# Kernel tuning notes

Hardware: AMD Instinct MI355X
Metric: run time of the kernel (lower is better)

The kernel has to match this reference:

```python
import jax, jax.numpy as jnp
import numpy as np

N = 250_000
E = 8_000_000
EPS = 1e-5


def _bn(x, gamma, beta):
    # BatchNorm1d in training mode: batch stats over dim 0, biased variance
    mu = x.mean(axis=0)
    var = x.var(axis=0)
    return (x - mu) * jax.lax.rsqrt(var + EPS) * gamma + beta


def setup_inputs() -> dict:
    key = jax.random.key(0)
    ks = jax.random.split(key, 24)
    f32 = jnp.float32
    inp = {
        'pos': jax.random.normal(ks[0], (N, 2), f32),
        'vel': jax.random.normal(ks[1], (N, 2), f32),
        'edge_index': jax.random.randint(ks[2], (2, E), 0, N, jnp.int32),
        'lin_in_w': jax.random.normal(ks[3], (4, 4), f32) * 0.5,
        'lin_in_b': jax.random.normal(ks[4], (4,), f32) * 0.1,
        'msg_w1': jax.random.normal(ks[5], (8, 8), f32) * 0.35,
        'msg_b1': jax.random.normal(ks[6], (8,), f32) * 0.1,
        'msg_g1': jax.random.uniform(ks[7], (8,), f32, 0.5, 1.5),
        'msg_be1': jax.random.normal(ks[8], (8,), f32) * 0.1,
        'msg_w2': jax.random.normal(ks[9], (8, 4), f32) * 0.35,
        'msg_b2': jax.random.normal(ks[10], (4,), f32) * 0.1,
        'msg_g2': jax.random.uniform(ks[11], (4,), f32, 0.5, 1.5),
        'msg_be2': jax.random.normal(ks[12], (4,), f32) * 0.1,
        'upd_w1': jax.random.normal(ks[13], (8, 8), f32) * 0.35,
        'upd_b1': jax.random.normal(ks[14], (8,), f32) * 0.1,
        'upd_g1': jax.random.uniform(ks[15], (8,), f32, 0.5, 1.5),
        'upd_be1': jax.random.normal(ks[16], (8,), f32) * 0.1,
        'upd_w2': jax.random.normal(ks[17], (8, 4), f32) * 0.35,
        'upd_b2': jax.random.normal(ks[18], (4,), f32) * 0.1,
        'upd_g2': jax.random.uniform(ks[19], (4,), f32, 0.5, 1.5),
        'upd_be2': jax.random.normal(ks[20], (4,), f32) * 0.1,
        'pred_w': jax.random.normal(ks[21], (4, 2), f32) * 0.5,
        'pred_b': jax.random.normal(ks[22], (2,), f32) * 0.1,
    }
    return inp


def reference(pos, vel, edge_index,
              lin_in_w, lin_in_b,
              msg_w1, msg_b1, msg_g1, msg_be1,
              msg_w2, msg_b2, msg_g2, msg_be2,
              upd_w1, upd_b1, upd_g1, upd_be1,
              upd_w2, upd_b2, upd_g2, upd_be2,
              pred_w, pred_b):
    n = pos.shape[0]
    # input projection: h = lin_in(cat(pos, vel))  -> [N, 4]
    h = jnp.concatenate([pos, vel], axis=-1) @ lin_in_w + lin_in_b

    # PyG source_to_target: j = source = edge_index[0], i = target = edge_index[1]
    src, dst = edge_index[0], edge_index[1]
    h_i = h[dst]  # [E, 4]
    h_j = h[src]  # [E, 4]

    # message MLP on cat(h_i, h_j): Linear->BN->Tanh->Linear->BN->Tanh
    m = jnp.concatenate([h_i, h_j], axis=-1)            # [E, 8]
    m = jnp.tanh(_bn(m @ msg_w1 + msg_b1, msg_g1, msg_be1))
    m = jnp.tanh(_bn(m @ msg_w2 + msg_b2, msg_g2, msg_be2))  # [E, 4]

    # zero out messages where h_i == h_j exactly (self-like edges)
    zero_diff = jnp.all(h_i == h_j, axis=1)             # [E]
    m = jnp.where(zero_diff[:, None], 0.0, m)

    # aggregate: scatter-add on first half, scatter-mean on second half
    add_out = jax.ops.segment_sum(m[:, :2], dst, num_segments=n)   # [N, 2]
    sum_out = jax.ops.segment_sum(m[:, 2:], dst, num_segments=n)   # [N, 2]
    cnt = jax.ops.segment_sum(jnp.ones((m.shape[0],), m.dtype), dst, num_segments=n)
    mean_out = sum_out / jnp.maximum(cnt, 1.0)[:, None]
    aggr = jnp.concatenate([add_out, mean_out], axis=1)  # [N, 4]

    # update MLP on cat(h, aggr)
    u = jnp.concatenate([h, aggr], axis=-1)              # [N, 8]
    u = jnp.tanh(_bn(u @ upd_w1 + upd_b1, upd_g1, upd_be1))
    u = jnp.tanh(_bn(u @ upd_w2 + upd_b2, upd_g2, upd_be2))  # [N, 4]

    return u @ pred_w + pred_b                           # [N, 2]
```

## Files before the change

kernel.cpp:

```cpp
#include <hip/hip_runtime.h>

#define EPSBN 1e-5f
#define NB 512
#define GB 256
#define CAP 18000

typedef float vf4 __attribute__((ext_vector_type(4)));
typedef _Float16 vh8 __attribute__((ext_vector_type(8)));
typedef _Float16 vh4 __attribute__((ext_vector_type(4)));
typedef unsigned int uint32;

__device__ __forceinline__ float ftanh(float x) {
    float e = __expf(2.0f * x);
    return 1.0f - 2.0f * __builtin_amdgcn_rcpf(e + 1.0f);
}

__device__ __forceinline__ float wave_sum(float v) {
#pragma unroll
    for (int off = 32; off > 0; off >>= 1) v += __shfl_down(v, off);
    return v;
}

__device__ __forceinline__ void z1_of(const float4 hi, const float4 hj,
                                      const float* __restrict__ w, const float* __restrict__ b,
                                      float* z) {
#pragma unroll
    for (int j = 0; j < 8; ++j) {
        z[j] = b[j]
             + hi.x * w[0 * 8 + j] + hi.y * w[1 * 8 + j] + hi.z * w[2 * 8 + j] + hi.w * w[3 * 8 + j]
             + hj.x * w[4 * 8 + j] + hj.y * w[5 * 8 + j] + hj.z * w[6 * 8 + j] + hj.w * w[7 * 8 + j];
    }
}

__device__ __forceinline__ void mat8x4(const float* u, const float* w,
                                       const float* b, float* z) {
#pragma unroll
    for (int c = 0; c < 4; ++c) {
        float t = b[c];
#pragma unroll
        for (int k = 0; k < 8; ++k) t += u[k] * w[k * 4 + c];
        z[c] = t;
    }
}

__device__ __forceinline__ void mat8x8(const float* u, const float* __restrict__ w,
                                       const float* __restrict__ b, float* z) {
#pragma unroll
    for (int j = 0; j < 8; ++j) {
        float t = b[j];
#pragma unroll
        for (int k = 0; k < 8; ++k) t += u[k] * w[k * 8 + j];
        z[j] = t;
    }
}

template <int NV, int NW>
__device__ __forceinline__ void block_reduce_atomics(float* a, float* __restrict__ sums) {
    __shared__ float red[NV * NW];
    int wid = threadIdx.x >> 6, lane = threadIdx.x & 63;
#pragma unroll
    for (int i = 0; i < NV; ++i) {
        float v = wave_sum(a[i]);
        if (lane == 0) red[i * NW + wid] = v;
    }
    __syncthreads();
    if (threadIdx.x < NV) {
        float v = 0.f;
#pragma unroll
        for (int k = 0; k < NW; ++k) v += red[threadIdx.x * NW + k];
        atomicAdd(&sums[threadIdx.x], v);
    }
}

__device__ __forceinline__ void fin_lds(const float* __restrict__ sums,
                                        const float* __restrict__ g, const float* __restrict__ be,
                                        int d, float inv, float* out) {
    int j = threadIdx.x;
    if (j < d) {
        float mu = sums[j] * inv;
        float var = sums[d + j] * inv - mu * mu;
        float s = g[j] * rsqrtf(var + EPSBN);
        out[j] = s;
        out[d + j] = be[j] - mu * s;
    }
    __syncthreads();
}

__device__ __forceinline__ void stats1_edge(float4 hi, float4 hj,
                                            const float* __restrict__ w1, const float* __restrict__ b1,
                                            float* a) {
    float z[8];
    z1_of(hi, hj, w1, b1, z);
#pragma unroll
    for (int j = 0; j < 8; ++j) { a[j] += z[j]; a[8 + j] += z[j] * z[j]; }
}

__device__ __forceinline__ vf4 z2_edge(float4 hi, float4 hj,
                                       const float* __restrict__ w1, const float* __restrict__ b1,
                                       const float* ss1,
                                       const float* __restrict__ w2, const float* __restrict__ b2) {
    float z[8], m1[8], z2[4];
    z1_of(hi, hj, w1, b1, z);
#pragma unroll
    for (int j = 0; j < 8; ++j) m1[j] = ftanh(z[j] * ss1[j] + ss1[8 + j]);
    mat8x4(m1, w2, b2, z2);
    vf4 r = {z2[0], z2[1], z2[2], z2[3]};
    return r;
}

__device__ __forceinline__ void stats2_edge(float4 hi, float4 hj,
                                            const float* __restrict__ w1, const float* __restrict__ b1,
                                            const float* ss1,
                                            const float* __restrict__ w2, const float* __restrict__ b2,
                                            float* a) {
    vf4 q = z2_edge(hi, hj, w1, b1, ss1, w2, b2);
    a[0] += q.x; a[4] += q.x * q.x;
    a[1] += q.y; a[5] += q.y * q.y;
    a[2] += q.z; a[6] += q.z * q.z;
    a[3] += q.w; a[7] += q.w * q.w;
}

__device__ __forceinline__ void m1_ofh(vf4 ziA, vf4 ziB, vh8 zjh, float* m1) {
    m1[0] = ftanh(ziA.x + (float)zjh[0]); m1[1] = ftanh(ziA.y + (float)zjh[1]);
    m1[2] = ftanh(ziA.z + (float)zjh[2]); m1[3] = ftanh(ziA.w + (float)zjh[3]);
    m1[4] = ftanh(ziB.x + (float)zjh[4]); m1[5] = ftanh(ziB.y + (float)zjh[5]);
    m1[6] = ftanh(ziB.z + (float)zjh[6]); m1[7] = ftanh(ziB.w + (float)zjh[7]);
}

__global__ __launch_bounds__(256) void k_h(const float* __restrict__ pos, const float* __restrict__ vel,
                                           const float* __restrict__ w, const float* __restrict__ b,
                                           float4* __restrict__ h, int n) {
    int i = blockIdx.x * blockDim.x + threadIdx.x;
    if (i >= n) return;
    float2 p = ((const float2*)pos)[i];
    float2 v = ((const float2*)vel)[i];
    float o[4];
#pragma unroll
    for (int d = 0; d < 4; ++d)
        o[d] = b[d] + p.x * w[0 * 4 + d] + p.y * w[1 * 4 + d] + v.x * w[2 * 4 + d] + v.y * w[3 * 4 + d];
    h[i] = make_float4(o[0], o[1], o[2], o[3]);
}

__global__ __launch_bounds__(256) void k_zt(const float4* __restrict__ h,
                                            const float* __restrict__ w1, const float* __restrict__ b1,
                                            vf4* __restrict__ zi, vf4* __restrict__ zj, int n) {
    int i = blockIdx.x * blockDim.x + threadIdx.x;
    if (i >= n) return;
    float4 hv = h[i];
    float zi8[8], zj8[8];
#pragma unroll
    for (int j = 0; j < 8; ++j) {
        zi8[j] = hv.x * w1[0 * 8 + j] + hv.y * w1[1 * 8 + j] + hv.z * w1[2 * 8 + j] + hv.w * w1[3 * 8 + j];
        zj8[j] = b1[j]
               + hv.x * w1[4 * 8 + j] + hv.y * w1[5 * 8 + j] + hv.z * w1[6 * 8 + j] + hv.w * w1[7 * 8 + j];
    }
    vf4 a = {zi8[0], zi8[1], zi8[2], zi8[3]};
    vf4 b_ = {zi8[4], zi8[5], zi8[6], zi8[7]};
    vf4 c = {zj8[0], zj8[1], zj8[2], zj8[3]};
    vf4 d = {zj8[4], zj8[5], zj8[6], zj8[7]};
    zi[2 * (size_t)i] = a; zi[2 * (size_t)i + 1] = b_;
    zj[2 * (size_t)i] = c; zj[2 * (size_t)i + 1] = d;
}

__global__ __launch_bounds__(256) void k_fold(vf4* __restrict__ zi, const vf4* __restrict__ zj,
                                              vh8* __restrict__ zjH,
                                              const float* __restrict__ sums1,
                                              const float* __restrict__ g1, const float* __restrict__ be1,
                                              float invE, int n) {
    __shared__ float ss1[16];
    fin_lds(sums1, g1, be1, 8, invE, ss1);
    int i = blockIdx.x * blockDim.x + threadIdx.x;
    if (i >= n) return;
    vf4 a = zi[2 * (size_t)i], b = zi[2 * (size_t)i + 1];
    a.x *= ss1[0]; a.y *= ss1[1]; a.z *= ss1[2]; a.w *= ss1[3];
    b.x *= ss1[4]; b.y *= ss1[5]; b.z *= ss1[6]; b.w *= ss1[7];
    zi[2 * (size_t)i] = a; zi[2 * (size_t)i + 1] = b;
    vf4 c = zj[2 * (size_t)i], d = zj[2 * (size_t)i + 1];
    vh8 hpk;
    hpk[0] = (_Float16)(c.x * ss1[0] + ss1[8]);
    hpk[1] = (_Float16)(c.y * ss1[1] + ss1[9]);
    hpk[2] = (_Float16)(c.z * ss1[2] + ss1[10]);
    hpk[3] = (_Float16)(c.w * ss1[3] + ss1[11]);
    hpk[4] = (_Float16)(d.x * ss1[4] + ss1[12]);
    hpk[5] = (_Float16)(d.y * ss1[5] + ss1[13]);
    hpk[6] = (_Float16)(d.z * ss1[6] + ss1[14]);
    hpk[7] = (_Float16)(d.w * ss1[7] + ss1[15]);
    zjH[i] = hpk;
}

__global__ __launch_bounds__(1024, 1) void k_cnt(const int* __restrict__ idx, const float4* __restrict__ h,
                                                 const float* __restrict__ w1, const float* __restrict__ b1,
                                                 uint32* __restrict__ cntmat, float* __restrict__ sums,
                                                 int E_, int T) {
    __shared__ uint32 hist[NB];
    for (int b = threadIdx.x; b < NB; b += 1024) hist[b] = 0;
    float a[16];
#pragma unroll
    for (int i = 0; i < 16; ++i) a[i] = 0.f;
    __syncthreads();
    int lo = blockIdx.x * T, hi2 = min(E_, lo + T);
    for (int e0 = lo + 4 * threadIdx.x; e0 < hi2; e0 += 4096) {
        int m = min(4, hi2 - e0);
        if (m == 4) {
            int s0 = __builtin_nontemporal_load(idx + e0);
            int s1 = __builtin_nontemporal_load(idx + e0 + 1);
            int s2 = __builtin_nontemporal_load(idx + e0 + 2);
            int s3 = __builtin_nontemporal_load(idx + e0 + 3);
            int d0 = __builtin_nontemporal_load(idx + E_ + e0);
            int d1 = __builtin_nontemporal_load(idx + E_ + e0 + 1);
            int d2 = __builtin_nontemporal_load(idx + E_ + e0 + 2);
            int d3 = __builtin_nontemporal_load(idx + E_ + e0 + 3);
            float4 hi0 = h[d0], hj0 = h[s0];
            float4 hi1 = h[d1], hj1 = h[s1];
            float4 hi2 = h[d2], hj2 = h[s2];
            float4 hi3 = h[d3], hj3 = h[s3];
            atomicAdd(&hist[d0 >> 9], 1u);
            atomicAdd(&hist[d1 >> 9], 1u);
            atomicAdd(&hist[d2 >> 9], 1u);
            atomicAdd(&hist[d3 >> 9], 1u);
            stats1_edge(hi0, hj0, w1, b1, a);
            stats1_edge(hi1, hj1, w1, b1, a);
            stats1_edge(hi2, hj2, w1, b1, a);
            stats1_edge(hi3, hj3, w1, b1, a);
        } else {
            for (int k = 0; k < m; ++k) {
                int s = __builtin_nontemporal_load(idx + e0 + k);
                int d = __builtin_nontemporal_load(idx + E_ + e0 + k);
                float4 hi = h[d], hj = h[s];
                atomicAdd(&hist[d >> 9], 1u);
                stats1_edge(hi, hj, w1, b1, a);
            }
        }
    }
    __syncthreads();
    for (int b = threadIdx.x; b < NB; b += 1024)
        cntmat[(size_t)b * GB + blockIdx.x] = hist[b];
    block_reduce_atomics<16, 16>(a, sums);
}

__device__ __forceinline__ void scan256(uint32 v, uint32* excl_out, uint32* total) {
    __shared__ uint32 ts[256];
    ts[threadIdx.x] = v;
    __syncthreads();
    for (int off = 1; off < 256; off <<= 1) {
        uint32 t = (threadIdx.x >= (uint32)off) ? ts[threadIdx.x - off] : 0u;
        __syncthreads();
        ts[threadIdx.x] += t;
        __syncthreads();
    }
    *excl_out = ts[threadIdx.x] - v;
    *total = ts[255];
}

__device__ __forceinline__ void scan512(uint32* v, uint32* excl_out, uint32* total) {
    __shared__ uint32 ts[256];
    uint32 local = v[0] + v[1];
    ts[threadIdx.x] = local;
    __syncthreads();
    for (int off = 1; off < 256; off <<= 1) {
        uint32 t = (threadIdx.x >= (uint32)off) ? ts[threadIdx.x - off] : 0u;
        __syncthreads();
        ts[threadIdx.x] += t;
        __syncthreads();
    }
    *excl_out = ts[threadIdx.x] - local;
    *total = ts[255];
}

__global__ __launch_bounds__(256) void k_scanA(uint32* __restrict__ cntmat, uint32* __restrict__ rowtot) {
    size_t base = (size_t)blockIdx.x * GB + threadIdx.x;
    uint32 v = cntmat[base];
    uint32 excl, tot;
    scan256(v, &excl, &tot);
    cntmat[base] = excl;
    if (threadIdx.x == 0) rowtot[blockIdx.x] = tot;
}

__global__ __launch_bounds__(256) void k_scanB(const uint32* __restrict__ rowtot, uint32* __restrict__ bbase) {
    uint32 v[2];
    v[0] = rowtot[threadIdx.x * 2]; v[1] = rowtot[threadIdx.x * 2 + 1];
    uint32 excl, tot;
    scan512(v, &excl, &tot);
    bbase[threadIdx.x * 2] = excl;
    bbase[threadIdx.x * 2 + 1] = excl + v[0];
    if (threadIdx.x == 0) bbase[NB] = tot;
}

__global__ __launch_bounds__(1024, 1) void k_reorder(const int* __restrict__ idx,
                                                     const uint32* __restrict__ cntmat, const uint32* __restrict__ bbase,
                                                     uint32* __restrict__ sp, int E_, int T) {
    __shared__ uint32 cur[NB];
    for (int b = threadIdx.x; b < NB; b += 1024)
        cur[b] = bbase[b] + cntmat[(size_t)b * GB + blockIdx.x];
    __syncthreads();
    int lo = blockIdx.x * T, hi2 = min(E_, lo + T);
    for (int e0 = lo + 4 * threadIdx.x; e0 < hi2; e0 += 4096) {
        int m = min(4, hi2 - e0);
        if (m == 4) {
            int s0 = __builtin_nontemporal_load(idx + e0);
            int s1 = __builtin_nontemporal_load(idx + e0 + 1);
            int s2 = __builtin_nontemporal_load(idx + e0 + 2);
            int s3 = __builtin_nontemporal_load(idx + e0 + 3);
            int d0 = __builtin_nontemporal_load(idx + E_ + e0);
            int d1 = __builtin_nontemporal_load(idx + E_ + e0 + 1);
            int d2 = __builtin_nontemporal_load(idx + E_ + e0 + 2);
            int d3 = __builtin_nontemporal_load(idx + E_ + e0 + 3);
            uint32 p0 = atomicAdd(&cur[d0 >> 9], 1u);
            uint32 p1 = atomicAdd(&cur[d1 >> 9], 1u);
            uint32 p2 = atomicAdd(&cur[d2 >> 9], 1u);
            uint32 p3 = atomicAdd(&cur[d3 >> 9], 1u);
            sp[p0] = ((uint32)(d0 & 511) << 23) | (uint32)s0;
            sp[p1] = ((uint32)(d1 & 511) << 23) | (uint32)s1;
            sp[p2] = ((uint32)(d2 & 511) << 23) | (uint32)s2;
            sp[p3] = ((uint32)(d3 & 511) << 23) | (uint32)s3;
        } else {
            for (int k = 0; k < m; ++k) {
                int s = __builtin_nontemporal_load(idx + e0 + k);
                int d = __builtin_nontemporal_load(idx + E_ + e0 + k);
                uint32 pos = atomicAdd(&cur[d >> 9], 1u);
                sp[pos] = ((uint32)(d & 511) << 23) | (uint32)s;
            }
        }
    }
}

__global__ __launch_bounds__(256) void k_sort2(const uint32* __restrict__ sp,
                                               const uint32* __restrict__ bbase, const uint32* __restrict__ rowtot,
                                               int* __restrict__ src2, uint32* __restrict__ nodeoff, int n) {
    extern __shared__ uint32 buf[];
    __shared__ uint32 hist[512];
    __shared__ uint32 cur[512];
    int b = blockIdx.x;
    uint32 start = bbase[b];
    uint32 len = rowtot[b];
    uint32 end = start + len;
    hist[threadIdx.x] = 0;
    hist[threadIdx.x + 256] = 0;
    __syncthreads();
    for (uint32 e = start + threadIdx.x; e < end; e += 256) {
        uint32 pk = __builtin_nontemporal_load(&sp[e]);
        atomicAdd(&hist[pk >> 23], 1u);
    }
    __syncthreads();
    uint32 vv[2];
    vv[0] = hist[2 * threadIdx.x];
    vv[1] = hist[2 * threadIdx.x + 1];
    uint32 excl, tot;
    scan512(vv, &excl, &tot);
    cur[2 * threadIdx.x] = excl;
    cur[2 * threadIdx.x + 1] = excl + vv[0];
    int nodebase = b << 9;
    int node0 = nodebase + 2 * threadIdx.x;
    if (node0 <= n)     nodeoff[node0] = start + excl;
    if (node0 + 1 <= n) nodeoff[node0 + 1] = start + excl + vv[0];
    __syncthreads();
    for (uint32 e = start + threadIdx.x; e < end; e += 256) {
        uint32 pk = __builtin_nontemporal_load(&sp[e]);
        uint32 pos = atomicAdd(&cur[pk >> 23], 1u);
        uint32 src = pk & 0x7FFFFFu;
        if (pos < (uint32)CAP) buf[pos] = src;
        else src2[start + pos] = (int)src;
    }
    __syncthreads();
    uint32 lim = min(len, (uint32)CAP);
    for (uint32 k = threadIdx.x; k < lim; k += 256)
        src2[start + k] = (int)buf[k];
}

__global__ void k_fin(const float* __restrict__ sums, float* __restrict__ ss,
                      const float* __restrict__ g, const float* __restrict__ be,
                      int d, float inv_count) {
    int j = threadIdx.x;
    if (j >= d) return;
    float mu = sums[j] * inv_count;
    float var = sums[d + j] * inv_count - mu * mu;
    float s = g[j] * rsqrtf(var + EPSBN);
    ss[j] = s;
    ss[d + j] = be[j] - mu * s;
}

__global__ __launch_bounds__(256, 2) void e_pass2(const int* __restrict__ src2, const uint32* __restrict__ nodeoff,
                                                  const vf4* __restrict__ ziS, const vh8* __restrict__ zjH,
                                                  const float* __restrict__ w2, const float* __restrict__ b2,
                                                  float* __restrict__ sums2, vh4* __restrict__ z2h, int n) {
    __shared__ float w2l[32];
    __shared__ float b2l[4];
    if (threadIdx.x < 32) w2l[threadIdx.x] = w2[threadIdx.x];
    if (threadIdx.x < 4)  b2l[threadIdx.x] = b2[threadIdx.x];
    __syncthreads();
    float a[8];
#pragma unroll
    for (int i = 0; i < 8; ++i) a[i] = 0.f;
    int lane = threadIdx.x & 15;
    int gid0 = (blockIdx.x * 256 + threadIdx.x) >> 4;
    int gstride = (gridDim.x * 256) >> 4;
    for (int i = gid0; i < n; i += gstride) {
        uint32 e0 = nodeoff[i], e1 = nodeoff[i + 1];
        vf4 ziA = ziS[2 * (size_t)i], ziB = ziS[2 * (size_t)i + 1];
        for (uint32 e = e0 + lane; e < e1; e += 16) {
            int s = src2[e];
            vh8 zjh = zjH[s];
            float m1[8], z2[4];
            m1_ofh(ziA, ziB, zjh, m1);
            mat8x4(m1, w2l, b2l, z2);
            a[0] += z2[0]; a[4] += z2[0] * z2[0];
            a[1] += z2[1]; a[5] += z2[1] * z2[1];
            a[2] += z2[2]; a[6] += z2[2] * z2[2];
            a[3] += z2[3]; a[7] += z2[3] * z2[3];
            vh4 pk;
            pk[0] = (s == i) ? (_Float16)__builtin_inff() : (_Float16)z2[0];
            pk[1] = (_Float16)z2[1];
            pk[2] = (_Float16)z2[2];
            pk[3] = (_Float16)z2[3];
            z2h[e] = pk;
        }
    }
    block_reduce_atomics<8, 4>(a, sums2);
}

__global__ __launch_bounds__(256, 2) void e_aggr_z(const vh4* __restrict__ z2h, const uint32* __restrict__ nodeoff,
                                                   const float* __restrict__ sums2,
                                                   const float* __restrict__ g2, const float* __restrict__ be2,
                                                   float invE,
                                                   float* __restrict__ acc, int n) {
    __shared__ float ss2[8];
    fin_lds(sums2, g2, be2, 4, invE, ss2);
    int lane = threadIdx.x & 15;
    int gid0 = (blockIdx.x * 256 + threadIdx.x) >> 4;
    int gstride = (gridDim.x * 256) >> 4;
    for (int i = gid0; i < n; i += gstride) {
        uint32 e0 = nodeoff[i], e1 = nodeoff[i + 1];
        float a0 = 0.f, a1 = 0.f, a2 = 0.f, a3 = 0.f;
        for (uint32 e = e0 + lane; e < e1; e += 16) {
            vh4 pk = z2h[e];
            float z0 = (float)pk[0];
            if (z0 != __builtin_inff()) {
                a0 += ftanh(z0 * ss2[0] + ss2[4]);
                a1 += ftanh((float)pk[1] * ss2[1] + ss2[5]);
                a2 += ftanh((float)pk[2] * ss2[2] + ss2[6]);
                a3 += ftanh((float)pk[3] * ss2[3] + ss2[7]);
            }
        }
#pragma unroll
        for (int off = 8; off > 0; off >>= 1) {
            a0 += __shfl_down(a0, off, 16);
            a1 += __shfl_down(a1, off, 16);
            a2 += __shfl_down(a2, off, 16);
            a3 += __shfl_down(a3, off, 16);
        }
        if (lane == 0) {
            float* ap = acc + 8 * (size_t)i;
            ap[0] = a0; ap[1] = a1; ap[2] = a2; ap[3] = a3;
            ap[4] = (float)(e1 - e0);
        }
    }
}

__global__ __launch_bounds__(256) void fb_stats1(const int* __restrict__ idx, const float4* __restrict__ h,
                                                 const float* __restrict__ w1, const float* __restrict__ b1,
                                                 float* __restrict__ sums, float* __restrict__ acc, int E_) {
    float a[16];
#pragma unroll
    for (int i = 0; i < 16; ++i) a[i] = 0.f;
    int stride = gridDim.x * blockDim.x;
    for (int e = blockIdx.x * blockDim.x + threadIdx.x; e < E_; e += stride) {
        int s = __builtin_nontemporal_load(idx + e);
        int d = __builtin_nontemporal_load(idx + E_ + e);
        float4 hi = h[d], hj = h[s];
        stats1_edge(hi, hj, w1, b1, a);
        atomicAdd(acc + 8 * (size_t)d + 4, 1.0f);
    }
    block_reduce_atomics<16, 4>(a, sums);
}

__global__ __launch_bounds__(256) void fb_stats2(const int* __restrict__ idx, const float4* __restrict__ h,
                                                 const float* __restrict__ w1, const float* __restrict__ b1,
                                                 const float* __restrict__ ss1,
                                                 const float* __restrict__ w2, const float* __restrict__ b2,
                                                 float* __restrict__ sums2, int E_) {
    float a[8];
#pragma unroll
    for (int i = 0; i < 8; ++i) a[i] = 0.f;
    int stride = gridDim.x * blockDim.x;
    for (int e = blockIdx.x * blockDim.x + threadIdx.x; e < E_; e += stride) {
        int s = __builtin_nontemporal_load(idx + e);
        int d = __builtin_nontemporal_load(idx + E_ + e);
        float4 hi = h[d], hj = h[s];
        stats2_edge(hi, hj, w1, b1, ss1, w2, b2, a);
    }
    block_reduce_atomics<8, 4>(a, sums2);
}

__global__ __launch_bounds__(256) void fb_scatter(const int* __restrict__ idx, const float4* __restrict__ h,
                                                  const float* __restrict__ w1, const float* __restrict__ b1,
                                                  const float* __restrict__ ss1,
                                                  const float* __restrict__ w2, const float* __restrict__ b2,
                                                  const float* __restrict__ ss2,
                                                  float* __restrict__ acc, int E_) {
    int stride = gridDim.x * blockDim.x;
    for (int e = blockIdx.x * blockDim.x + threadIdx.x; e < E_; e += stride) {
        int s = __builtin_nontemporal_load(idx + e);
        int d = __builtin_nontemporal_load(idx + E_ + e);
        float4 hi = h[d], hj = h[s];
        bool zero = (hi.x == hj.x) && (hi.y == hj.y) && (hi.z == hj.z) && (hi.w == hj.w);
        if (zero) continue;
        vf4 q = z2_edge(hi, hj, w1, b1, ss1, w2, b2);
        float m0 = ftanh(q.x * ss2[0] + ss2[4]);
        float m1v = ftanh(q.y * ss2[1] + ss2[5]);
        float m2v = ftanh(q.z * ss2[2] + ss2[6]);
        float m3 = ftanh(q.w * ss2[3] + ss2[7]);
        float* ap = acc + 8 * (size_t)d;
        atomicAdd(ap + 0, m0);
        atomicAdd(ap + 1, m1v);
        atomicAdd(ap + 2, m2v);
        atomicAdd(ap + 3, m3);
    }
}

__device__ __forceinline__ void load_u(int i, const float4* __restrict__ h,
                                       const float* __restrict__ acc, float* u) {
    float4 hv = h[i];
    const float* ap = acc + 8 * (size_t)i;
    float c = fmaxf(ap[4], 1.0f);
    u[0] = hv.x; u[1] = hv.y; u[2] = hv.z; u[3] = hv.w;
    u[4] = ap[0]; u[5] = ap[1]; u[6] = ap[2] / c; u[7] = ap[3] / c;
}

__global__ __launch_bounds__(256) void n_stats1(const float4* __restrict__ h,
                                                const float* __restrict__ acc,
                                                const float* __restrict__ w, const float* __restrict__ b,
                                                float* __restrict__ sums, int n) {
    float a[16];
#pragma unroll
    for (int i = 0; i < 16; ++i) a[i] = 0.f;
    int stride = gridDim.x * blockDim.x;
    for (int i = blockIdx.x * blockDim.x + threadIdx.x; i < n; i += stride) {
        float u[8], z[8];
        load_u(i, h, acc, u);
        mat8x8(u, w, b, z);
#pragma unroll
        for (int j = 0; j < 8; ++j) { a[j] += z[j]; a[8 + j] += z[j] * z[j]; }
    }
    block_reduce_atomics<16, 4>(a, sums);
}

__global__ __launch_bounds__(256) void n_stats2(const float4* __restrict__ h,
                                                const float* __restrict__ acc,
                                                const float* __restrict__ w1, const float* __restrict__ b1,
                                                const float* __restrict__ sums3,
                                                const float* __restrict__ g3, const float* __restrict__ be3,
                                                float invN,
                                                const float* __restrict__ w2, const float* __restrict__ b2,
                                                float* __restrict__ sums, int n) {
    __shared__ float ss3[16];
    fin_lds(sums3, g3, be3, 8, invN, ss3);
    float a[8];
#pragma unroll
    for (int i = 0; i < 8; ++i) a[i] = 0.f;
    int stride = gridDim.x * blockDim.x;
    for (int i = blockIdx.x * blockDim.x + threadIdx.x; i < n; i += stride) {
        float u[8], z[8], u1[8], z4[4];
        load_u(i, h, acc, u);
        mat8x8(u, w1, b1, z);
#pragma unroll
        for (int j = 0; j < 8; ++j) u1[j] = ftanh(z[j] * ss3[j] + ss3[8 + j]);
        mat8x4(u1, w2, b2, z4);
#pragma unroll
        for (int c = 0; c < 4; ++c) { a[c] += z4[c]; a[4 + c] += z4[c] * z4[c]; }
    }
    block_reduce_atomics<8, 4>(a, sums);
}

__global__ __launch_bounds__(256) void n_final(const float4* __restrict__ h,
                                               const float* __restrict__ acc,
                                               const float* __restrict__ w1, const float* __restrict__ b1,
                                               const float* __restrict__ sums3,
                                               const float* __restrict__ g3, const float* __restrict__ be3,
                                               const float* __restrict__ sums4,
                                               const float* __restrict__ g4, const float* __restrict__ be4,
                                               float invN,
                                               const float* __restrict__ w2, const float* __restrict__ b2,
                                               const float* __restrict__ pw, const float* __restrict__ pb,
                                               float2* __restrict__ out, int n) {
    __shared__ float ss3[16];
    __shared__ float ss4[8];
    fin_lds(sums3, g3, be3, 8, invN, ss3);
    fin_lds(sums4, g4, be4, 4, invN, ss4);
    int stride = gridDim.x * blockDim.x;
    for (int i = blockIdx.x * blockDim.x + threadIdx.x; i < n; i += stride) {
        float u[8], z[8], u1[8], z4[4], u2[4];
        load_u(i, h, acc, u);
        mat8x8(u, w1, b1, z);
#pragma unroll
        for (int j = 0; j < 8; ++j) u1[j] = ftanh(z[j] * ss3[j] + ss3[8 + j]);
        mat8x4(u1, w2, b2, z4);
#pragma unroll
        for (int c = 0; c < 4; ++c) u2[c] = ftanh(z4[c] * ss4[c] + ss4[4 + c]);
        float o0 = pb[0] + u2[0] * pw[0] + u2[1] * pw[2] + u2[2] * pw[4] + u2[3] * pw[6];
        float o1 = pb[1] + u2[0] * pw[1] + u2[1] * pw[3] + u2[2] * pw[5] + u2[3] * pw[7];
        out[i] = make_float2(o0, o1);
    }
}

extern "C" void kernel_launch(void* const* d_in, const int* in_sizes, int n_in,
                              void* d_out, int out_size, void* d_ws, size_t ws_size,
                              hipStream_t stream) {
    const float* pos  = (const float*)d_in[0];
    const float* vel  = (const float*)d_in[1];
    const int*   eidx = (const int*)d_in[2];
    const float* lin_w = (const float*)d_in[3];
    const float* lin_b = (const float*)d_in[4];
    const float* mw1 = (const float*)d_in[5];
    const float* mb1 = (const float*)d_in[6];
    const float* mg1 = (const float*)d_in[7];
    const float* mbe1 = (const float*)d_in[8];
    const float* mw2 = (const float*)d_in[9];
    const float* mb2 = (const float*)d_in[10];
    const float* mg2 = (const float*)d_in[11];
    const float* mbe2 = (const float*)d_in[12];
    const float* uw1 = (const float*)d_in[13];
    const float* ub1 = (const float*)d_in[14];
    const float* ug1 = (const float*)d_in[15];
    const float* ube1 = (const float*)d_in[16];
    const float* uw2 = (const float*)d_in[17];
    const float* ub2 = (const float*)d_in[18];
    const float* ug2 = (const float*)d_in[19];
    const float* ube2 = (const float*)d_in[20];
    const float* pw = (const float*)d_in[21];
    const float* pb = (const float*)d_in[22];

    int n  = in_sizes[0] / 2;
    int E_ = in_sizes[2] / 2;
    float invE = 1.0f / (float)E_;
    float invN = 1.0f / (float)n;

    char* base = (char*)d_ws;
    size_t off = 0;
    auto alloc = [&](size_t bytes) {
        off = (off + 15) & ~(size_t)15;
        void* p = base + off;
        off += bytes;
        return p;
    };
    float4* h       = (float4*)alloc(16 * (size_t)n);
    float*  acc     = (float*)alloc(32 * (size_t)n);
    float*  sums    = (float*)alloc(512);
    float*  ss      = sums + 64;
    uint32* bbase   = (uint32*)alloc(4 * (NB + 1));
    uint32* rowtot  = (uint32*)alloc(4 * NB);
    uint32* cntmat  = (uint32*)alloc(4 * (size_t)NB * GB);
    uint32* nodeoff = (uint32*)alloc(4 * ((size_t)n + 1));
    vf4*    ziS     = (vf4*)alloc(32 * (size_t)n);
    vf4*    zjS     = (vf4*)alloc(32 * (size_t)n);
    vh8*    zjH     = (vh8*)alloc(16 * (size_t)n);
    int*    src2    = (int*)alloc(4 * (size_t)E_);
    uint32* sp      = (uint32*)alloc(4 * (size_t)E_);
    vh4*    z2h     = (vh4*)alloc(8 * (size_t)E_);
    size_t need_sort = off;

    bool big = (ws_size >= need_sort) && (n < (1 << 23));

    int nblk = (n + 255) / 256;
    int nbuckets = (n + 511) >> 9;
    int T = (E_ + GB - 1) / GB;

    k_h<<<nblk, 256, 0, stream>>>(pos, vel, lin_w, lin_b, h, n);

    if (big) {
        (void)hipMemsetAsync(sums, 0, 256, stream);

        k_zt<<<nblk, 256, 0, stream>>>(h, mw1, mb1, ziS, zjS, n);

        k_cnt<<<GB, 1024, 0, stream>>>(eidx, h, mw1, mb1, cntmat, sums, E_, T);
        k_scanA<<<NB, 256, 0, stream>>>(cntmat, rowtot);
        k_scanB<<<1, 256, 0, stream>>>(rowtot, bbase);

        k_fold<<<nblk, 256, 0, stream>>>(ziS, zjS, zjH, sums, mg1, mbe1, invE, n);

        k_reorder<<<GB, 1024, 0, stream>>>(eidx, cntmat, bbase, sp, E_, T);
        k_sort2<<<nbuckets, 256, CAP * 4, stream>>>(sp, bbase, rowtot, src2, nodeoff, n);

        e_pass2<<<4096, 256, 0, stream>>>(src2, nodeoff, ziS, zjH, mw2, mb2, sums + 16, z2h, n);

        e_aggr_z<<<4096, 256, 0, stream>>>(z2h, nodeoff, sums + 16, mg2, mbe2, invE, acc, n);

        n_stats1<<<nblk, 256, 0, stream>>>(h, acc, uw1, ub1, sums + 24, n);
        n_stats2<<<nblk, 256, 0, stream>>>(h, acc, uw1, ub1, sums + 24, ug1, ube1, invN,
                                           uw2, ub2, sums + 40, n);
        n_final<<<nblk, 256, 0, stream>>>(h, acc, uw1, ub1, sums + 24, ug1, ube1,
                                          sums + 40, ug2, ube2, invN,
                                          uw2, ub2, pw, pb, (float2*)d_out, n);
    } else {
        (void)hipMemsetAsync(acc, 0, 32 * (size_t)n + 256, stream);

        fb_stats1<<<4096, 256, 0, stream>>>(eidx, h, mw1, mb1, sums, acc, E_);
        k_fin<<<1, 64, 0, stream>>>(sums, ss, mg1, mbe1, 8, invE);

        fb_stats2<<<4096, 256, 0, stream>>>(eidx, h, mw1, mb1, ss, mw2, mb2, sums + 16, E_);
        k_fin<<<1, 64, 0, stream>>>(sums + 16, ss + 16, mg2, mbe2, 4, invE);

        fb_scatter<<<4096, 256, 0, stream>>>(eidx, h, mw1, mb1, ss, mw2, mb2, ss + 16, acc, E_);

        n_stats1<<<nblk, 256, 0, stream>>>(h, acc, uw1, ub1, sums + 24, n);
        n_stats2<<<nblk, 256, 0, stream>>>(h, acc, uw1, ub1, sums + 24, ug1, ube1, invN,
                                           uw2, ub2, sums + 40, n);
        n_final<<<nblk, 256, 0, stream>>>(h, acc, uw1, ub1, sums + 24, ug1, ube1,
                                          sums + 40, ug2, ube2, invN,
                                          uw2, ub2, pw, pb, (float2*)d_out, n);
    }
}
```

Baseline: 412.3 us.

## Compute first BN stats from sorted CSR via decomposed sums, slim count pass

The first message-layer BatchNorm statistics move out of the edge-order histogram kernel, which gathered h for both endpoints of every edge. They are now computed after sorting, per destination node. The sums split algebraically into a zi part weighted by node degree and per-node sums over gathered half-precision zj, plus a cross term. The count kernel now reads only dst indices, and zj is stored directly as unnormalized fp16 with the BN scale/shift applied inside e_pass2. The cost is an extra CSR pass and fp16 rounding of the pre-normalization zj. The fallback path also gains an odd inline extern declaration and a stray k_fin1 call.

```diff
diff --git a/kernel.cpp b/kernel.cpp
--- a/kernel.cpp
+++ b/kernel.cpp
@@ -120,13 +120,6 @@
     a[3] += q.w; a[7] += q.w * q.w;
 }
 
-__device__ __forceinline__ void m1_ofh(vf4 ziA, vf4 ziB, vh8 zjh, float* m1) {
-    m1[0] = ftanh(ziA.x + (float)zjh[0]); m1[1] = ftanh(ziA.y + (float)zjh[1]);
-    m1[2] = ftanh(ziA.z + (float)zjh[2]); m1[3] = ftanh(ziA.w + (float)zjh[3]);
-    m1[4] = ftanh(ziB.x + (float)zjh[4]); m1[5] = ftanh(ziB.y + (float)zjh[5]);
-    m1[6] = ftanh(ziB.z + (float)zjh[6]); m1[7] = ftanh(ziB.w + (float)zjh[7]);
-}
-
 __global__ __launch_bounds__(256) void k_h(const float* __restrict__ pos, const float* __restrict__ vel,
                                            const float* __restrict__ w, const float* __restrict__ b,
                                            float4* __restrict__ h, int n) {
@@ -143,99 +136,52 @@
 
 __global__ __launch_bounds__(256) void k_zt(const float4* __restrict__ h,
                                             const float* __restrict__ w1, const float* __restrict__ b1,
-                                            vf4* __restrict__ zi, vf4* __restrict__ zj, int n) {
+                                            vf4* __restrict__ zi, vh8* __restrict__ zjH, int n) {
     int i = blockIdx.x * blockDim.x + threadIdx.x;
     if (i >= n) return;
     float4 hv = h[i];
-    float zi8[8], zj8[8];
+    float zi8[8];
+    vh8 hpk;
 #pragma unroll
     for (int j = 0; j < 8; ++j) {
         zi8[j] = hv.x * w1[0 * 8 + j] + hv.y * w1[1 * 8 + j] + hv.z * w1[2 * 8 + j] + hv.w * w1[3 * 8 + j];
-        zj8[j] = b1[j]
-               + hv.x * w1[4 * 8 + j] + hv.y * w1[5 * 8 + j] + hv.z * w1[6 * 8 + j] + hv.w * w1[7 * 8 + j];
+        float zj = b1[j]
+                 + hv.x * w1[4 * 8 + j] + hv.y * w1[5 * 8 + j] + hv.z * w1[6 * 8 + j] + hv.w * w1[7 * 8 + j];
+        hpk[j] = (_Float16)zj;
     }
     vf4 a = {zi8[0], zi8[1], zi8[2], zi8[3]};
     vf4 b_ = {zi8[4], zi8[5], zi8[6], zi8[7]};
-    vf4 c = {zj8[0], zj8[1], zj8[2], zj8[3]};
-    vf4 d = {zj8[4], zj8[5], zj8[6], zj8[7]};
     zi[2 * (size_t)i] = a; zi[2 * (size_t)i + 1] = b_;
-    zj[2 * (size_t)i] = c; zj[2 * (size_t)i + 1] = d;
-}
-
-__global__ __launch_bounds__(256) void k_fold(vf4* __restrict__ zi, const vf4* __restrict__ zj,
-                                              vh8* __restrict__ zjH,
-                                              const float* __restrict__ sums1,
-                                              const float* __restrict__ g1, const float* __restrict__ be1,
-                                              float invE, int n) {
-    __shared__ float ss1[16];
-    fin_lds(sums1, g1, be1, 8, invE, ss1);
-    int i = blockIdx.x * blockDim.x + threadIdx.x;
-    if (i >= n) return;
-    vf4 a = zi[2 * (size_t)i], b = zi[2 * (size_t)i + 1];
-    a.x *= ss1[0]; a.y *= ss1[1]; a.z *= ss1[2]; a.w *= ss1[3];
-    b.x *= ss1[4]; b.y *= ss1[5]; b.z *= ss1[6]; b.w *= ss1[7];
-    zi[2 * (size_t)i] = a; zi[2 * (size_t)i + 1] = b;
-    vf4 c = zj[2 * (size_t)i], d = zj[2 * (size_t)i + 1];
-    vh8 hpk;
-    hpk[0] = (_Float16)(c.x * ss1[0] + ss1[8]);
-    hpk[1] = (_Float16)(c.y * ss1[1] + ss1[9]);
-    hpk[2] = (_Float16)(c.z * ss1[2] + ss1[10]);
-    hpk[3] = (_Float16)(c.w * ss1[3] + ss1[11]);
-    hpk[4] = (_Float16)(d.x * ss1[4] + ss1[12]);
-    hpk[5] = (_Float16)(d.y * ss1[5] + ss1[13]);
-    hpk[6] = (_Float16)(d.z * ss1[6] + ss1[14]);
-    hpk[7] = (_Float16)(d.w * ss1[7] + ss1[15]);
     zjH[i] = hpk;
 }
 
-__global__ __launch_bounds__(1024, 1) void k_cnt(const int* __restrict__ idx, const float4* __restrict__ h,
-                                                 const float* __restrict__ w1, const float* __restrict__ b1,
-                                                 uint32* __restrict__ cntmat, float* __restrict__ sums,
+__global__ __launch_bounds__(1024, 1) void k_cnt(const int* __restrict__ dst, uint32* __restrict__ cntmat,
                                                  int E_, int T) {
     __shared__ uint32 hist[NB];
     for (int b = threadIdx.x; b < NB; b += 1024) hist[b] = 0;
-    float a[16];
-#pragma unroll
-    for (int i = 0; i < 16; ++i) a[i] = 0.f;
     __syncthreads();
     int lo = blockIdx.x * T, hi2 = min(E_, lo + T);
     for (int e0 = lo + 4 * threadIdx.x; e0 < hi2; e0 += 4096) {
         int m = min(4, hi2 - e0);
         if (m == 4) {
-            int s0 = __builtin_nontemporal_load(idx + e0);
-            int s1 = __builtin_nontemporal_load(idx + e0 + 1);
-            int s2 = __builtin_nontemporal_load(idx + e0 + 2);
-            int s3 = __builtin_nontemporal_load(idx + e0 + 3);
-            int d0 = __builtin_nontemporal_load(idx + E_ + e0);
-            int d1 = __builtin_nontemporal_load(idx + E_ + e0 + 1);
-            int d2 = __builtin_nontemporal_load(idx + E_ + e0 + 2);
-            int d3 = __builtin_nontemporal_load(idx + E_ + e0 + 3);
-            float4 hi0 = h[d0], hj0 = h[s0];
-            float4 hi1 = h[d1], hj1 = h[s1];
-            float4 hi2 = h[d2], hj2 = h[s2];
-            float4 hi3 = h[d3], hj3 = h[s3];
+            int d0 = __builtin_nontemporal_load(dst + e0);
+            int d1 = __builtin_nontemporal_load(dst + e0 + 1);
+            int d2 = __builtin_nontemporal_load(dst + e0 + 2);
+            int d3 = __builtin_nontemporal_load(dst + e0 + 3);
             atomicAdd(&hist[d0 >> 9], 1u);
             atomicAdd(&hist[d1 >> 9], 1u);
             atomicAdd(&hist[d2 >> 9], 1u);
             atomicAdd(&hist[d3 >> 9], 1u);
-            stats1_edge(hi0, hj0, w1, b1, a);
-            stats1_edge(hi1, hj1, w1, b1, a);
-            stats1_edge(hi2, hj2, w1, b1, a);
-            stats1_edge(hi3, hj3, w1, b1, a);
         } else {
             for (int k = 0; k < m; ++k) {
-                int s = __builtin_nontemporal_load(idx + e0 + k);
-                int d = __builtin_nontemporal_load(idx + E_ + e0 + k);
-                float4 hi = h[d], hj = h[s];
+                int d = __builtin_nontemporal_load(dst + e0 + k);
                 atomicAdd(&hist[d >> 9], 1u);
-                stats1_edge(hi, hj, w1, b1, a);
             }
         }
     }
     __syncthreads();
     for (int b = threadIdx.x; b < NB; b += 1024)
         cntmat[(size_t)b * GB + blockIdx.x] = hist[b];
-    block_reduce_atomics<16, 16>(a, sums);
 }
 
 __device__ __forceinline__ void scan256(uint32 v, uint32* excl_out, uint32* total) {
@@ -367,26 +313,84 @@
         src2[start + k] = (int)buf[k];
 }
 
-__global__ void k_fin(const float* __restrict__ sums, float* __restrict__ ss,
-                      const float* __restrict__ g, const float* __restrict__ be,
-                      int d, float inv_count) {
-    int j = threadIdx.x;
-    if (j >= d) return;
-    float mu = sums[j] * inv_count;
-    float var = sums[d + j] * inv_count - mu * mu;
-    float s = g[j] * rsqrtf(var + EPSBN);
-    ss[j] = s;
-    ss[d + j] = be[j] - mu * s;
+__global__ __launch_bounds__(256, 2) void e_stats1(const int* __restrict__ src2, const uint32* __restrict__ nodeoff,
+                                                   const vf4* __restrict__ ziS, const vh8* __restrict__ zjH,
+                                                   float* __restrict__ sums, int n) {
+    float a[40];
+#pragma unroll
+    for (int i = 0; i < 40; ++i) a[i] = 0.f;
+    int lane = threadIdx.x & 15;
+    int gid0 = (blockIdx.x * 256 + threadIdx.x) >> 4;
+    int gstride = (gridDim.x * 256) >> 4;
+    for (int i = gid0; i < n; i += gstride) {
+        uint32 e0 = nodeoff[i], e1 = nodeoff[i + 1];
+        vf4 ziA = ziS[2 * (size_t)i], ziB = ziS[2 * (size_t)i + 1];
+        float zi8[8] = {ziA.x, ziA.y, ziA.z, ziA.w, ziB.x, ziB.y, ziB.z, ziB.w};
+        float t1[8], t2[8];
+#pragma unroll
+        for (int c = 0; c < 8; ++c) { t1[c] = 0.f; t2[c] = 0.f; }
+        int cnt = 0;
+        for (uint32 e = e0 + lane; e < e1; e += 16) {
+            int s = src2[e];
+            vh8 zjh = zjH[s];
+#pragma unroll
+            for (int c = 0; c < 8; ++c) {
+                float zj = (float)zjh[c];
+                t1[c] += zj;
+                t2[c] += zj * zj;
+            }
+            cnt++;
+        }
+        float fc = (float)cnt;
+#pragma unroll
+        for (int c = 0; c < 8; ++c) {
+            a[c]      += fc * zi8[c];
+            a[8 + c]  += fc * zi8[c] * zi8[c];
+            a[16 + c] += t1[c];
+            a[24 + c] += t2[c];
+            a[32 + c] += zi8[c] * t1[c];
+        }
+    }
+    block_reduce_atomics<40, 4>(a, sums);
+}
+
+__global__ void k_fin1(const float* __restrict__ sums,
+                       const float* __restrict__ g1, const float* __restrict__ be1,
+                       float invE, float* __restrict__ ss1g) {
+    int c = threadIdx.x;
+    if (c >= 8) return;
+    float S1 = sums[c] + sums[16 + c];
+    float S2 = sums[8 + c] + 2.0f * sums[32 + c] + sums[24 + c];
+    float mu = S1 * invE;
+    float var = S2 * invE - mu * mu;
+    float s = g1[c] * rsqrtf(var + EPSBN);
+    ss1g[c] = s;
+    ss1g[8 + c] = be1[c] - mu * s;
+}
+
+__global__ __launch_bounds__(256) void k_fold(vf4* __restrict__ zi, const float* __restrict__ ss1g, int n) {
+    __shared__ float s[8];
+    if (threadIdx.x < 8) s[threadIdx.x] = ss1g[threadIdx.x];
+    __syncthreads();
+    int i = blockIdx.x * blockDim.x + threadIdx.x;
+    if (i >= n) return;
+    vf4 a = zi[2 * (size_t)i], b = zi[2 * (size_t)i + 1];
+    a.x *= s[0]; a.y *= s[1]; a.z *= s[2]; a.w *= s[3];
+    b.x *= s[4]; b.y *= s[5]; b.z *= s[6]; b.w *= s[7];
+    zi[2 * (size_t)i] = a; zi[2 * (size_t)i + 1] = b;
 }
 
 __global__ __launch_bounds__(256, 2) void e_pass2(const int* __restrict__ src2, const uint32* __restrict__ nodeoff,
                                                   const vf4* __restrict__ ziS, const vh8* __restrict__ zjH,
+                                                  const float* __restrict__ ss1g,
                                                   const float* __restrict__ w2, const float* __restrict__ b2,
                                                   float* __restrict__ sums2, vh4* __restrict__ z2h, int n) {
     __shared__ float w2l[32];
     __shared__ float b2l[4];
+    __shared__ float st[16];
     if (threadIdx.x < 32) w2l[threadIdx.x] = w2[threadIdx.x];
     if (threadIdx.x < 4)  b2l[threadIdx.x] = b2[threadIdx.x];
+    if (threadIdx.x < 16) st[threadIdx.x] = ss1g[threadIdx.x];
     __syncthreads();
     float a[8];
 #pragma unroll
@@ -397,11 +401,14 @@
     for (int i = gid0; i < n; i += gstride) {
         uint32 e0 = nodeoff[i], e1 = nodeoff[i + 1];
         vf4 ziA = ziS[2 * (size_t)i], ziB = ziS[2 * (size_t)i + 1];
+        float zi8[8] = {ziA.x, ziA.y, ziA.z, ziA.w, ziB.x, ziB.y, ziB.z, ziB.w};
         for (uint32 e = e0 + lane; e < e1; e += 16) {
             int s = src2[e];
             vh8 zjh = zjH[s];
             float m1[8], z2[4];
-            m1_ofh(ziA, ziB, zjh, m1);
+#pragma unroll
+            for (int c = 0; c < 8; ++c)
+                m1[c] = ftanh(zi8[c] + st[c] * (float)zjh[c] + st[8 + c]);
             mat8x4(m1, w2l, b2l, z2);
             a[0] += z2[0]; a[4] += z2[0] * z2[0];
             a[1] += z2[1]; a[5] += z2[1] * z2[1];
@@ -646,12 +653,12 @@
     float*  acc     = (float*)alloc(32 * (size_t)n);
     float*  sums    = (float*)alloc(512);
     float*  ss      = sums + 64;
+    float*  ss1g    = (float*)alloc(256);
     uint32* bbase   = (uint32*)alloc(4 * (NB + 1));
     uint32* rowtot  = (uint32*)alloc(4 * NB);
     uint32* cntmat  = (uint32*)alloc(4 * (size_t)NB * GB);
     uint32* nodeoff = (uint32*)alloc(4 * ((size_t)n + 1));
     vf4*    ziS     = (vf4*)alloc(32 * (size_t)n);
-    vf4*    zjS     = (vf4*)alloc(32 * (size_t)n);
     vh8*    zjH     = (vh8*)alloc(16 * (size_t)n);
     int*    src2    = (int*)alloc(4 * (size_t)E_);
     uint32* sp      = (uint32*)alloc(4 * (size_t)E_);
@@ -667,22 +674,45 @@
     k_h<<<nblk, 256, 0, stream>>>(pos, vel, lin_w, lin_b, h, n);
 
     if (big) {
-        (void)hipMemsetAsync(sums, 0, 256, stream);
-
-        k_zt<<<nblk, 256, 0, stream>>>(h, mw1, mb1, ziS, zjS, n);
-
-        k_cnt<<<GB, 1024, 0, stream>>>(eidx, h, mw1, mb1, cntmat, sums, E_, T);
+        (void)hipMemsetAsync(sums, 0, 512, stream);
+
+        k_zt<<<nblk, 256, 0, stream>>>(h, mw1, mb1, ziS, zjH, n);
+
+        k_cnt<<<GB, 1024, 0, stream>>>(eidx + E_, cntmat, E_, T);
         k_scanA<<<NB, 256, 0, stream>>>(cntmat, rowtot);
         k_scanB<<<1, 256, 0, stream>>>(rowtot, bbase);
 
-        k_fold<<<nblk, 256, 0, stream>>>(ziS, zjS, zjH, sums, mg1, mbe1, invE, n);
-
         k_reorder<<<GB, 1024, 0, stream>>>(eidx, cntmat, bbase, sp, E_, T);
         k_sort2<<<nbuckets, 256, CAP * 4, stream>>>(sp, bbase, rowtot, src2, nodeoff, n);
 
-        e_pass2<<<4096, 256, 0, stream>>>(src2, nodeoff, ziS, zjH, mw2, mb2, sums + 16, z2h, n);
-
-        e_aggr_z<<<4096, 256, 0, stream>>>(z2h, nodeoff, sums + 16, mg2, mbe2, invE, acc, n);
+        e_stats1<<<4096, 256, 0, stream>>>(src2, nodeoff, ziS, zjH, sums, n);
+        k_fin1<<<1, 64, 0, stream>>>(sums, mg1, mbe1, invE, ss1g);
+        k_fold<<<nblk, 256, 0, stream>>>(ziS, ss1g, n);
+
+        e_pass2<<<4096, 256, 0, stream>>>(src2, nodeoff, ziS, zjH, ss1g,
+                                          mw2, mb2, sums + 40, z2h, n);
+
+        e_aggr_z<<<4096, 256, 0, stream>>>(z2h, nodeoff, sums + 40, mg2, mbe2, invE, acc, n);
+
+        n_stats1<<<nblk, 256, 0, stream>>>(h, acc, uw1, ub1, sums + 48, n);
+        n_stats2<<<nblk, 256, 0, stream>>>(h, acc, uw1, ub1, sums + 48, ug1, ube1, invN,
+                                           uw2, ub2, sums + 64, n);
+        n_final<<<nblk, 256, 0, stream>>>(h, acc, uw1, ub1, sums + 48, ug1, ube1,
+                                          sums + 64, ug2, ube2, invN,
+                                          uw2, ub2, pw, pb, (float2*)d_out, n);
+    } else {
+        (void)hipMemsetAsync(acc, 0, 32 * (size_t)n + 256, stream);
+        (void)hipMemsetAsync(sums, 0, 512, stream);
+
+        fb_stats1<<<4096, 256, 0, stream>>>(eidx, h, mw1, mb1, sums, acc, E_);
+        k_fin1<<<1, 64, 0, stream>>>(sums, mg1, mbe1, invE, ss1g);
+        {
+        }
+        extern __global__ void k_fin(const float*, float*, const float*, const float*, int, float);
+        k_fin<<<1, 64, 0, stream>>>(sums, ss, mg1, mbe1, 8, invE);
+        fb_stats2<<<4096, 256, 0, stream>>>(eidx, h, mw1, mb1, ss, mw2, mb2, sums + 16, E_);
+        k_fin<<<1, 64, 0, stream>>>(sums + 16, ss + 16, mg2, mbe2, 4, invE);
+        fb_scatter<<<4096, 256, 0, stream>>>(eidx, h, mw1, mb1, ss, mw2, mb2, ss + 16, acc, E_);
 
         n_stats1<<<nblk, 256, 0, stream>>>(h, acc, uw1, ub1, sums + 24, n);
         n_stats2<<<nblk, 256, 0, stream>>>(h, acc, uw1, ub1, sums + 24, ug1, ube1, invN,
@@ -690,22 +720,17 @@
         n_final<<<nblk, 256, 0, stream>>>(h, acc, uw1, ub1, sums + 24, ug1, ube1,
                                           sums + 40, ug2, ube2, invN,
                                           uw2, ub2, pw, pb, (float2*)d_out, n);
-    } else {
-        (void)hipMemsetAsync(acc, 0, 32 * (size_t)n + 256, stream);
-
-        fb_stats1<<<4096, 256, 0, stream>>>(eidx, h, mw1, mb1, sums, acc, E_);
-        k_fin<<<1, 64, 0, stream>>>(sums, ss, mg1, mbe1, 8, invE);
-
-        fb_stats2<<<4096, 256, 0, stream>>>(eidx, h, mw1, mb1, ss, mw2, mb2, sums + 16, E_);
-        k_fin<<<1, 64, 0, stream>>>(sums + 16, ss + 16, mg2, mbe2, 4, invE);
-
-        fb_scatter<<<4096, 256, 0, stream>>>(eidx, h, mw1, mb1, ss, mw2, mb2, ss + 16, acc, E_);
-
-        n_stats1<<<nblk, 256, 0, stream>>>(h, acc, uw1, ub1, sums + 24, n);
-        n_stats2<<<nblk, 256, 0, stream>>>(h, acc, uw1, ub1, sums + 24, ug1, ube1, invN,
-                                           uw2, ub2, sums + 40, n);
-        n_final<<<nblk, 256, 0, stream>>>(h, acc, uw1, ub1, sums + 24, ug1, ube1,
-                                          sums + 40, ug2, ube2, invN,
-                                          uw2, ub2, pw, pb, (float2*)d_out, n);
-    }
-}
+    }
+}
+
+__global__ void k_fin(const float* __restrict__ sums, float* __restrict__ ss,
+                      const float* __restrict__ g, const float* __restrict__ be,
+                      int d, float inv_count) {
+    int j = threadIdx.x;
+    if (j >= d) return;
+    float mu = sums[j] * inv_count;
+    float var = sums[d + j] * inv_count - mu * mu;
+    float s = g[j] * rsqrtf(var + EPSBN);
+    ss[j] = s;
+    ss[d + j] = be[j] - mu * s;
+}
```

After: 478.1 us. +16.0%, slower.
